# Kernel optimization log

Measured on AMD Instinct MI355X. Metric: run time of the kernel, lower is better.

The kernel has to match this reference:

```python
import jax, jax.numpy as jnp
import numpy as np

N_NODES = 50000
N_EDGES = 800000
NF = 64       # input_nf = output_nf = hidden_nf
RADIAL = 1

def tanhshrink(x):
    return x - jnp.tanh(x)

def _linear_params(key, fan_in, fan_out):
    k1, k2 = jax.random.split(key)
    s = 1.0 / np.sqrt(fan_in)
    W = jax.random.uniform(k1, (fan_in, fan_out), jnp.float32, -s, s)
    b = jax.random.uniform(k2, (fan_out,), jnp.float32, -s, s)
    return W, b

def setup_inputs() -> dict:
    key = jax.random.key(0)
    ks = jax.random.split(key, 11)
    nodes = jax.random.normal(ks[0], (N_NODES, NF), jnp.float32)
    coord = jax.random.normal(ks[1], (N_NODES, 3), jnp.float32)
    edges = jax.random.randint(ks[2], (2, N_EDGES), 0, N_NODES, jnp.int64)
    # Edge MLP: Linear(2*NF + RADIAL -> NF), Linear(NF -> NF)
    eW1, eb1 = _linear_params(ks[3], 2 * NF + RADIAL, NF)
    eW2, eb2 = _linear_params(ks[4], NF, NF)
    # Edge attention: Linear(2*NF -> NF), Linear(NF -> 1)
    aW1, ab1 = _linear_params(ks[5], 2 * NF, NF)
    aW2, ab2 = _linear_params(ks[6], NF, 1)
    # Node MLP: Linear(NF + NF -> NF), Linear(NF -> NF)
    nW1, nb1 = _linear_params(ks[7], 2 * NF, NF)
    nW2, nb2 = _linear_params(ks[8], NF, NF)
    # Coord MLP: Linear(NF -> NF), Linear(NF -> 1)
    cW1, cb1 = _linear_params(ks[9], NF, NF)
    cW2, cb2 = _linear_params(ks[10], NF, 1)
    return dict(nodes=nodes, coord=coord, edges=edges,
                eW1=eW1, eb1=eb1, eW2=eW2, eb2=eb2,
                aW1=aW1, ab1=ab1, aW2=aW2, ab2=ab2,
                nW1=nW1, nb1=nb1, nW2=nW2, nb2=nb2,
                cW1=cW1, cb1=cb1, cW2=cW2, cb2=cb2)

def reference(nodes, coord, edges,
              eW1, eb1, eW2, eb2,
              aW1, ab1, aW2, ab2,
              nW1, nb1, nW2, nb2,
              cW1, cb1, cW2, cb2):
    row, col = edges[0], edges[1]
    n = nodes.shape[0]
    # Radial: squared distance along each edge
    rij = coord[row] - coord[col]                       # [E, 3]
    radial = jnp.sum(rij * rij, axis=1, keepdims=True)  # [E, 1]
    src, tgt = nodes[row], nodes[col]                   # [E, NF]
    # Edge MLP with attention gate
    agg_in = jnp.concatenate([src, tgt, radial], axis=1)
    h = tanhshrink(agg_in @ eW1 + eb1)
    h = tanhshrink(h @ eW2 + eb2)                       # [E, NF]
    att_in = jnp.concatenate([src, tgt], axis=1)
    a = tanhshrink(att_in @ aW1 + ab1)
    a = jax.nn.sigmoid(a @ aW2 + ab2)                   # [E, 1]
    edge_feat = h * a                                   # [E, NF]
    # Coordinate update: rij scaled by scalar per edge, scatter-add to row
    c = tanhshrink(edge_feat @ cW1 + cb1)
    trans = rij * (c @ cW2 + cb2)                       # [E, 3]
    coord_out = coord + jax.ops.segment_sum(trans, row, num_segments=n)
    # Node update: scatter-add edge features to row, residual MLP
    agg = jax.ops.segment_sum(edge_feat, row, num_segments=n)  # [N, NF]
    m = jnp.concatenate([nodes, agg], axis=1)
    m = tanhshrink(m @ nW1 + nb1)
    nodes_out = nodes + (m @ nW2 + nb2)
    return nodes_out, coord_out
```

## Files before the change

### kernel.cpp

```cpp
#include <hip/hip_runtime.h>
#include <hip/hip_fp16.h>

#define NF 64

typedef _Float16 half8 __attribute__((ext_vector_type(8)));
typedef float f32x4 __attribute__((ext_vector_type(4)));

__device__ __forceinline__ float ts_f(float x){
  float t = __expf(2.0f*x);
  float th = 1.0f - 2.0f*__builtin_amdgcn_rcpf(t + 1.0f);
  return x - th;
}
__device__ __forceinline__ float sigmoid_f(float x){
  return __builtin_amdgcn_rcpf(1.0f + __expf(-x));
}

__global__ __launch_bounds__(256) void k_prepw_hist(
    const float* __restrict__ eW1, const float* __restrict__ aW1,
    const float* __restrict__ eW2, const float* __restrict__ cW1,
    const float* __restrict__ nW1, const float* __restrict__ nW2,
    _Float16* __restrict__ W256t, _Float16* __restrict__ N1t,
    _Float16* __restrict__ W2t, _Float16* __restrict__ C1t,
    _Float16* __restrict__ N2t,
    const int* __restrict__ edges, int* __restrict__ counts, int E)
{
  const int bi = blockIdx.x;
  if (bi < 64){
    const int t = bi*256 + threadIdx.x;
    {
      const int n = t >> 6, k = t & 63;
      float v;
      if      (n < 64)  v = eW1[k*NF + n];
      else if (n < 128) v = aW1[k*NF + (n-64)];
      else if (n < 192) v = eW1[(64+k)*NF + (n-128)];
      else              v = aW1[(64+k)*NF + (n-192)];
      W256t[t] = (_Float16)v;
    }
    if (t < 64*128){
      const int n = t >> 7, k = t & 127;
      N1t[t] = (_Float16)nW1[k*NF + n];
    }
    if (t < 64*64){
      const int n = t >> 6, k = t & 63;
      W2t[t] = (_Float16)eW2[k*NF + n];
      C1t[t] = (_Float16)cW1[k*NF + n];
      N2t[t] = (_Float16)nW2[k*NF + n];
    }
  } else {
    const int e = (bi - 64)*256 + threadIdx.x;
    if (e < E) atomicAdd(&counts[edges[e]], 1);
  }
}

__global__ __launch_bounds__(256) void k_scan(
    const int* __restrict__ counts, int* __restrict__ offs,
    int* __restrict__ btot, int* __restrict__ btop, int* __restrict__ done)
{
  __shared__ int s[256];
  __shared__ int isLast;
  const int t = threadIdx.x;
  const int b = blockIdx.x;

  const int4 c = *(const int4*)(counts + b*1024 + 4*t);
  const int mysum = c.x + c.y + c.z + c.w;
  s[t] = mysum; __syncthreads();
  #pragma unroll
  for (int d=1; d<256; d<<=1){
    const int v = (t>=d) ? s[t-d] : 0; __syncthreads();
    s[t] += v; __syncthreads();
  }
  const int base = (t==0) ? 0 : s[t-1];
  int4 o;
  o.x = base; o.y = base + c.x; o.z = o.y + c.y; o.w = o.z + c.z;
  *(int4*)(offs + b*1024 + 4*t) = o;
  if (t == 255) btot[b] = s[255];

  __threadfence();
  if (t == 0) isLast = (atomicAdd(done, 1) == (int)gridDim.x - 1);
  __syncthreads();
  if (isLast){
    __threadfence();
    const int nb = gridDim.x;
    const int v = (t < nb) ? btot[t] : 0;
    s[t] = v; __syncthreads();
    #pragma unroll
    for (int d=1; d<256; d<<=1){
      const int u = (t>=d) ? s[t-d] : 0; __syncthreads();
      s[t] += u; __syncthreads();
    }
    if (t < nb) btop[t] = (t==0) ? 0 : s[t-1];
  }
}

__global__ __launch_bounds__(64, 8) void k_pre_scatter(
    const float* __restrict__ nodes,
    const float* __restrict__ eb1, const float* __restrict__ ab1,
    const _Float16* __restrict__ W256t,
    _Float16* __restrict__ P, _Float16* __restrict__ Q, int N,
    const int* __restrict__ edges, int* __restrict__ offs,
    const int* __restrict__ btop, int2* __restrict__ ecomb, int E,
    int preBlocks)
{
  const int bi = blockIdx.x;
  const int lane = threadIdx.x;
  if (bi >= preBlocks){
    const int e = (bi - preBlocks)*64 + lane;
    if (e < E){
      const int r = edges[e], c = edges[E + e];
      const int pos = btop[r >> 10] + atomicAdd(&offs[r], 1);
      ecomb[pos] = make_int2(r, c);
    }
    return;
  }

  const int p = lane & 15, q = lane >> 4;
  const int m0 = bi * 16;
  const int row = m0 + p;

  const float* __restrict__ xr = nodes + (size_t)row * NF;
  half8 A[2];
  #pragma unroll
  for (int kt=0; kt<2; kt++){
    const float4 xa = *(const float4*)(xr + kt*32 + q*8);
    const float4 xb = *(const float4*)(xr + kt*32 + q*8 + 4);
    A[kt][0]=(_Float16)xa.x; A[kt][1]=(_Float16)xa.y; A[kt][2]=(_Float16)xa.z; A[kt][3]=(_Float16)xa.w;
    A[kt][4]=(_Float16)xb.x; A[kt][5]=(_Float16)xb.y; A[kt][6]=(_Float16)xb.z; A[kt][7]=(_Float16)xb.w;
  }

  #pragma unroll
  for (int ni=0; ni<16; ni++){
    float b = 0.f;
    if (ni < 4)       b = eb1[16*ni + p];
    else if (ni < 8)  b = ab1[16*(ni-4) + p];
    f32x4 acc = (f32x4){b,b,b,b};
    #pragma unroll
    for (int kt=0; kt<2; kt++){
      const half8 Bf = *(const half8*)(W256t + (size_t)(16*ni + p)*NF + kt*32 + q*8);
      acc = __builtin_amdgcn_mfma_f32_16x16x32_f16(A[kt], Bf, acc, 0,0,0);
    }
    _Float16* __restrict__ dst = (ni < 8 ? P : Q);
    const int colbase = (ni & 7) * 16 + p;
    #pragma unroll
    for (int rr=0; rr<4; rr++)
      dst[(size_t)(m0 + 4*q + rr)*128 + colbase] = (_Float16)acc[rr];
  }
}

__global__ __launch_bounds__(64, 4) void egcl_edge(
    const float* __restrict__ coord,
    const int2*  __restrict__ ecomb,
    const _Float16* __restrict__ P, const _Float16* __restrict__ Q,
    const float* __restrict__ eW1,
    const _Float16* __restrict__ W2t, const float* __restrict__ eb2,
    const float* __restrict__ aW2, const float* __restrict__ ab2,
    const _Float16* __restrict__ C1t, const float* __restrict__ cb1,
    const float* __restrict__ cW2, const float* __restrict__ cb2,
    _Float16* __restrict__ aggh, float* __restrict__ coord_out,
    int E)
{
  __shared__ _Float16 tile[64][72];
  __shared__ float gbuf[64];
  __shared__ float csbuf[64];
  __shared__ float tbuf[64][4];
  __shared__ int   rbuf[64];

  const int lane = threadIdx.x;
  const int p = lane & 15, q = lane >> 4;
  const int e = blockIdx.x * 64 + lane;
  const bool valid = (e < E);
  const int el = valid ? e : (E - 1);

  const int2 e2 = ecomb[el];
  const int r = e2.x, c = e2.y;
  rbuf[lane] = valid ? r : -1;

  const float rx = coord[3*r+0] - coord[3*c+0];
  const float ry = coord[3*r+1] - coord[3*c+1];
  const float rz = coord[3*r+2] - coord[3*c+2];
  const float radial = rx*rx + ry*ry + rz*rz;

  const _Float16* __restrict__ Pr = P + (size_t)r * 128;
  const _Float16* __restrict__ Qc = Q + (size_t)c * 128;
  const float* __restrict__ wrad = eW1 + 128*NF;

  half8 Bf[4][2];
  #pragma unroll
  for (int ni=0;ni<4;ni++)
    #pragma unroll
    for (int kt=0;kt<2;kt++)
      Bf[ni][kt] = *(const half8*)(W2t + (size_t)(16*ni + p)*NF + kt*32 + q*8);

  float sp0=0.f, sp1=0.f;
  #pragma unroll
  for (int g=0;g<8;g++){
    const half8 pa = *(const half8*)(Pr + 64 + 8*g);
    const half8 qa = *(const half8*)(Qc + 64 + 8*g);
    #pragma unroll
    for (int j=0;j<8;j++){
      const float v = ts_f((float)pa[j] + (float)qa[j]);
      if (j & 1) sp1 = fmaf(v, aW2[8*g+j], sp1); else sp0 = fmaf(v, aW2[8*g+j], sp0);
    }
  }
  const float gate = sigmoid_f(sp0 + sp1 + ab2[0]);
  gbuf[lane] = gate;

  #pragma unroll
  for (int g=0;g<8;g++){
    const half8 ph = *(const half8*)(Pr + 8*g);
    const half8 qh = *(const half8*)(Qc + 8*g);
    half8 hv;
    #pragma unroll
    for (int j=0;j<8;j++)
      hv[j] = (_Float16)ts_f(fmaf(radial, wrad[8*g+j], (float)ph[j] + (float)qh[j]));
    *(half8*)&tile[lane][8*g] = hv;
  }
  __syncthreads();

  f32x4 acc[4][4];
  #pragma unroll
  for (int ni=0;ni<4;ni++){
    const float b = eb2[16*ni + p];
    #pragma unroll
    for (int mi=0;mi<4;mi++) acc[mi][ni] = (f32x4){b,b,b,b};
  }
  #pragma unroll
  for (int mi=0;mi<4;mi++){
    #pragma unroll
    for (int kt=0;kt<2;kt++){
      const half8 Af = *(const half8*)&tile[16*mi + p][kt*32 + q*8];
      #pragma unroll
      for (int ni=0;ni<4;ni++)
        acc[mi][ni] = __builtin_amdgcn_mfma_f32_16x16x32_f16(Af, Bf[ni][kt], acc[mi][ni], 0,0,0);
    }
  }
  __syncthreads();

  #pragma unroll
  for (int mi=0;mi<4;mi++){
    #pragma unroll
    for (int rr=0;rr<4;rr++){
      const int row = 16*mi + 4*q + rr;
      const float gv = gbuf[row];
      #pragma unroll
      for (int ni=0;ni<4;ni++)
        tile[row][16*ni + p] = (_Float16)(ts_f(acc[mi][ni][rr]) * gv);
    }
  }

  #pragma unroll
  for (int ni=0;ni<4;ni++)
    #pragma unroll
    for (int kt=0;kt<2;kt++)
      Bf[ni][kt] = *(const half8*)(C1t + (size_t)(16*ni + p)*NF + kt*32 + q*8);
  #pragma unroll
  for (int ni=0;ni<4;ni++){
    const float b = cb1[16*ni + p];
    #pragma unroll
    for (int mi=0;mi<4;mi++) acc[mi][ni] = (f32x4){b,b,b,b};
  }
  __syncthreads();
  #pragma unroll
  for (int mi=0;mi<4;mi++){
    #pragma unroll
    for (int kt=0;kt<2;kt++){
      const half8 Af = *(const half8*)&tile[16*mi + p][kt*32 + q*8];
      #pragma unroll
      for (int ni=0;ni<4;ni++)
        acc[mi][ni] = __builtin_amdgcn_mfma_f32_16x16x32_f16(Af, Bf[ni][kt], acc[mi][ni], 0,0,0);
    }
  }

  float part[4][4];
  {
    float w2c[4];
    #pragma unroll
    for (int ni=0;ni<4;ni++) w2c[ni] = cW2[16*ni + p];
    #pragma unroll
    for (int mi=0;mi<4;mi++)
      #pragma unroll
      for (int rr=0;rr<4;rr++){
        float s = 0.f;
        #pragma unroll
        for (int ni=0;ni<4;ni++) s = fmaf(ts_f(acc[mi][ni][rr]), w2c[ni], s);
        part[mi][rr] = s;
      }
  }
  #pragma unroll
  for (int mask=1; mask<16; mask<<=1)
    #pragma unroll
    for (int mi=0;mi<4;mi++)
      #pragma unroll
      for (int rr=0;rr<4;rr++)
        part[mi][rr] += __shfl_xor(part[mi][rr], mask);
  {
    float v = 0.f;
    #pragma unroll
    for (int mi=0;mi<4;mi++)
      #pragma unroll
      for (int rr=0;rr<4;rr++)
        if (((p>>2)==mi) & ((p&3)==rr)) v = part[mi][rr];
    csbuf[16*(p>>2) + 4*q + (p&3)] = v + cb2[0];
  }
  __syncthreads();

  {
    const float cse = csbuf[lane];
    tbuf[lane][0] = rx * cse;
    tbuf[lane][1] = ry * cse;
    tbuf[lane][2] = rz * cse;
  }
  __syncthreads();

  {
    int cur = rbuf[0];
    float runsum = 0.f, rc = 0.f;
    #pragma unroll 1
    for (int eo=0; eo<64; eo++){
      const int rr2 = rbuf[eo];
      if (rr2 != cur){
        const float v0 = __shfl(runsum, 2*lane);
        const float v1 = __shfl(runsum, 2*lane+1);
        if (cur >= 0){
          if (lane < 32){
            __half2 hv; hv.x = __float2half(v0); hv.y = __float2half(v1);
            unsafeAtomicAdd((__half2*)aggh + (size_t)cur*32 + lane, hv);
          }
          if (lane < 3) atomicAdd(coord_out + 3*cur + lane, rc);
        }
        runsum = 0.f; rc = 0.f; cur = rr2;
      }
      runsum += (float)tile[eo][lane];
      if (lane < 3) rc += tbuf[eo][lane];
    }
    const float v0 = __shfl(runsum, 2*lane);
    const float v1 = __shfl(runsum, 2*lane+1);
    if (cur >= 0){
      if (lane < 32){
        __half2 hv; hv.x = __float2half(v0); hv.y = __float2half(v1);
        unsafeAtomicAdd((__half2*)aggh + (size_t)cur*32 + lane, hv);
      }
      if (lane < 3) atomicAdd(coord_out + 3*cur + lane, rc);
    }
  }
}

__global__ __launch_bounds__(64, 8) void egcl_node(
    const float* __restrict__ nodes, const float* __restrict__ coord,
    const _Float16* __restrict__ aggh,
    const _Float16* __restrict__ N1t, const float* __restrict__ nb1,
    const _Float16* __restrict__ N2t, const float* __restrict__ nb2,
    float* __restrict__ out_nodes, float* __restrict__ out_coord, int N)
{
  __shared__ _Float16 t2[16][72];
  const int lane = threadIdx.x;
  const int p = lane & 15, q = lane >> 4;
  const int m0 = blockIdx.x * 16;
  const int row = m0 + p;

  half8 A[4];
  const float* __restrict__ xr = nodes + (size_t)row * NF;
  #pragma unroll
  for (int kt=0; kt<2; kt++){
    const float4 xa = *(const float4*)(xr + kt*32 + q*8);
    const float4 xb = *(const float4*)(xr + kt*32 + q*8 + 4);
    A[kt][0]=(_Float16)xa.x; A[kt][1]=(_Float16)xa.y; A[kt][2]=(_Float16)xa.z; A[kt][3]=(_Float16)xa.w;
    A[kt][4]=(_Float16)xb.x; A[kt][5]=(_Float16)xb.y; A[kt][6]=(_Float16)xb.z; A[kt][7]=(_Float16)xb.w;
  }
  const _Float16* __restrict__ ar = aggh + (size_t)row * NF;
  #pragma unroll
  for (int kt=2; kt<4; kt++)
    A[kt] = *(const half8*)(ar + (kt-2)*32 + q*8);

  f32x4 acc[4];
  #pragma unroll
  for (int ni=0;ni<4;ni++){
    const float b = nb1[16*ni + p];
    acc[ni] = (f32x4){b,b,b,b};
  }
  #pragma unroll
  for (int kt=0; kt<4; kt++){
    #pragma unroll
    for (int ni=0;ni<4;ni++){
      const half8 Bf = *(const half8*)(N1t + (size_t)(16*ni + p)*128 + kt*32 + q*8);
      acc[ni] = __builtin_amdgcn_mfma_f32_16x16x32_f16(A[kt], Bf, acc[ni], 0,0,0);
    }
  }

  #pragma unroll
  for (int ni=0;ni<4;ni++)
    #pragma unroll
    for (int rr=0;rr<4;rr++)
      t2[4*q + rr][16*ni + p] = (_Float16)ts_f(acc[ni][rr]);
  __syncthreads();

  half8 A2[2];
  #pragma unroll
  for (int kt=0; kt<2; kt++)
    A2[kt] = *(const half8*)&t2[p][kt*32 + q*8];

  f32x4 acc2[4];
  #pragma unroll
  for (int ni=0;ni<4;ni++){
    const float b = nb2[16*ni + p];
    acc2[ni] = (f32x4){b,b,b,b};
  }
  #pragma unroll
  for (int kt=0; kt<2; kt++){
    #pragma unroll
    for (int ni=0;ni<4;ni++){
      const half8 Bf = *(const half8*)(N2t + (size_t)(16*ni + p)*NF + kt*32 + q*8);
      acc2[ni] = __builtin_amdgcn_mfma_f32_16x16x32_f16(A2[kt], Bf, acc2[ni], 0,0,0);
    }
  }

  #pragma unroll
  for (int ni=0;ni<4;ni++){
    #pragma unroll
    for (int rr=0;rr<4;rr++){
      const size_t idx = (size_t)(m0 + 4*q + rr)*NF + 16*ni + p;
      out_nodes[idx] = nodes[idx] + acc2[ni][rr];
    }
  }

  if (lane < 48)
    out_coord[(size_t)m0*3 + lane] += coord[(size_t)m0*3 + lane];
}

extern "C" void kernel_launch(void* const* d_in, const int* in_sizes, int n_in,
                              void* d_out, int out_size, void* d_ws, size_t ws_size,
                              hipStream_t stream)
{
  const float* nodes = (const float*)d_in[0];
  const float* coord = (const float*)d_in[1];
  const int*   edges = (const int*)  d_in[2];
  const float* eW1 = (const float*)d_in[3];
  const float* eb1 = (const float*)d_in[4];
  const float* eW2 = (const float*)d_in[5];
  const float* eb2 = (const float*)d_in[6];
  const float* aW1 = (const float*)d_in[7];
  const float* ab1 = (const float*)d_in[8];
  const float* aW2 = (const float*)d_in[9];
  const float* ab2 = (const float*)d_in[10];
  const float* nW1 = (const float*)d_in[11];
  const float* nb1 = (const float*)d_in[12];
  const float* nW2 = (const float*)d_in[13];
  const float* nb2 = (const float*)d_in[14];
  const float* cW1 = (const float*)d_in[15];
  const float* cb1 = (const float*)d_in[16];
  const float* cW2 = (const float*)d_in[17];
  const float* cb2 = (const float*)d_in[18];

  const int E = in_sizes[2] / 2;
  const int N = in_sizes[0] / NF;
  const int SCAN_B = (N + 1023) >> 10;
  const int NBINS  = SCAN_B << 10;
  float* out_nodes = (float*)d_out;
  float* out_coord = out_nodes + (size_t)N * NF;

  char* w = (char*)d_ws;
  _Float16* P     = (_Float16*)w;  w += (size_t)N * 128 * 2;
  _Float16* Qh    = (_Float16*)w;  w += (size_t)N * 128 * 2;
  char* zbase = w;
  _Float16* aggh  = (_Float16*)w;  w += (size_t)N * 64 * 2;
  int* counts     = (int*)w;       w += (size_t)NBINS * 4;
  int* done       = (int*)w;       w += 256;
  const size_t zlen = (size_t)(w - zbase);
  int* offs       = (int*)w;       w += (size_t)NBINS * 4;
  int* btot       = (int*)w;       w += 256*4;
  int* btop       = (int*)w;       w += 256*4;
  int2* ecomb     = (int2*)w;      w += (size_t)E * 8;
  _Float16* W256t = (_Float16*)w;  w += 256*64*2;
  _Float16* N1t   = (_Float16*)w;  w += 64*128*2;
  _Float16* W2t   = (_Float16*)w;  w += 64*64*2;
  _Float16* C1t   = (_Float16*)w;  w += 64*64*2;
  _Float16* N2t   = (_Float16*)w;  w += 64*64*2;

  hipMemsetAsync(out_coord, 0, (size_t)N * 3 * sizeof(float), stream);
  hipMemsetAsync(zbase, 0, zlen, stream);

  const int histBlocks = (E + 255)/256;
  k_prepw_hist<<<64 + histBlocks, 256, 0, stream>>>(eW1, aW1, eW2, cW1, nW1, nW2,
      W256t, N1t, W2t, C1t, N2t, edges, counts, E);

  k_scan<<<SCAN_B, 256, 0, stream>>>(counts, offs, btot, btop, done);

  const int preBlocks = (N + 15)/16;
  const int scatBlocks = (E + 63)/64;
  k_pre_scatter<<<preBlocks + scatBlocks, 64, 0, stream>>>(nodes, eb1, ab1, W256t,
      P, Qh, N, edges, offs, btop, ecomb, E, preBlocks);

  egcl_edge<<<(E + 63)/64, 64, 0, stream>>>(coord, ecomb, P, Qh,
      eW1, W2t, eb2, aW2, ab2, C1t, cb1, cW2, cb2,
      aggh, out_coord, E);

  egcl_node<<<(N + 15)/16, 64, 0, stream>>>(nodes, coord, aggh,
      N1t, nb1, N2t, nb2, out_nodes, out_coord, N);
}
```

Measured before the change: 343.4 us.

## Reuse histogram atomic ranks for edge scatter and fold zeroing into scan

The histogram pass now records each edge's atomicAdd return value as its rank within its row. The scatter pass then computes the sorted position as block offset + row offset + rank, with no second contended atomic. The aggregation buffer and coord_out are zeroed by extra blocks of the scan kernel instead of a separate memset. The sorted edge list is also split from int2 into separate row and column arrays. The cost is an extra E-sized rank array that must be written and read back.

Result: faster. 305.5 us (-11.1%).

```diff
diff --git a/kernel.cpp b/kernel.cpp
--- a/kernel.cpp
+++ b/kernel.cpp
@@ -22,7 +22,8 @@
     _Float16* __restrict__ W256t, _Float16* __restrict__ N1t,
     _Float16* __restrict__ W2t, _Float16* __restrict__ C1t,
     _Float16* __restrict__ N2t,
-    const int* __restrict__ edges, int* __restrict__ counts, int E)
+    const int* __restrict__ edges, int* __restrict__ counts,
+    int* __restrict__ rank, int E)
 {
   const int bi = blockIdx.x;
   if (bi < 64){
@@ -48,19 +49,30 @@
     }
   } else {
     const int e = (bi - 64)*256 + threadIdx.x;
-    if (e < E) atomicAdd(&counts[edges[e]], 1);
-  }
-}
-
-__global__ __launch_bounds__(256) void k_scan(
+    if (e < E) rank[e] = atomicAdd(&counts[edges[e]], 1);
+  }
+}
+
+__global__ __launch_bounds__(256) void k_scan_zero(
     const int* __restrict__ counts, int* __restrict__ offs,
-    int* __restrict__ btot, int* __restrict__ btop, int* __restrict__ done)
+    int* __restrict__ btot, int* __restrict__ btop, int* __restrict__ done,
+    float4* __restrict__ zagg, int naggf4,
+    float4* __restrict__ zcoord, int ncoordf4,
+    int SCAN_B)
 {
+  const int t = threadIdx.x;
+  const int b = blockIdx.x;
+  if (b >= SCAN_B){
+    const float4 z = make_float4(0.f,0.f,0.f,0.f);
+    const int nthr = (gridDim.x - SCAN_B) * 256;
+    const int tid = (b - SCAN_B)*256 + t;
+    for (int i = tid; i < naggf4; i += nthr)   zagg[i] = z;
+    for (int i = tid; i < ncoordf4; i += nthr) zcoord[i] = z;
+    return;
+  }
+
   __shared__ int s[256];
   __shared__ int isLast;
-  const int t = threadIdx.x;
-  const int b = blockIdx.x;
-
   const int4 c = *(const int4*)(counts + b*1024 + 4*t);
   const int mysum = c.x + c.y + c.z + c.w;
   s[t] = mysum; __syncthreads();
@@ -76,19 +88,18 @@
   if (t == 255) btot[b] = s[255];
 
   __threadfence();
-  if (t == 0) isLast = (atomicAdd(done, 1) == (int)gridDim.x - 1);
+  if (t == 0) isLast = (atomicAdd(done, 1) == SCAN_B - 1);
   __syncthreads();
   if (isLast){
     __threadfence();
-    const int nb = gridDim.x;
-    const int v = (t < nb) ? btot[t] : 0;
+    const int v = (t < SCAN_B) ? btot[t] : 0;
     s[t] = v; __syncthreads();
     #pragma unroll
     for (int d=1; d<256; d<<=1){
       const int u = (t>=d) ? s[t-d] : 0; __syncthreads();
       s[t] += u; __syncthreads();
     }
-    if (t < nb) btop[t] = (t==0) ? 0 : s[t-1];
+    if (t < SCAN_B) btop[t] = (t==0) ? 0 : s[t-1];
   }
 }
 
@@ -97,8 +108,9 @@
     const float* __restrict__ eb1, const float* __restrict__ ab1,
     const _Float16* __restrict__ W256t,
     _Float16* __restrict__ P, _Float16* __restrict__ Q, int N,
-    const int* __restrict__ edges, int* __restrict__ offs,
-    const int* __restrict__ btop, int2* __restrict__ ecomb, int E,
+    const int* __restrict__ edges, const int* __restrict__ offs,
+    const int* __restrict__ btop, const int* __restrict__ rank,
+    int* __restrict__ rs, int* __restrict__ cs, int E,
     int preBlocks)
 {
   const int bi = blockIdx.x;
@@ -107,8 +119,8 @@
     const int e = (bi - preBlocks)*64 + lane;
     if (e < E){
       const int r = edges[e], c = edges[E + e];
-      const int pos = btop[r >> 10] + atomicAdd(&offs[r], 1);
-      ecomb[pos] = make_int2(r, c);
+      const int pos = btop[r >> 10] + offs[r] + rank[e];
+      rs[pos] = r; cs[pos] = c;
     }
     return;
   }
@@ -148,7 +160,7 @@
 
 __global__ __launch_bounds__(64, 4) void egcl_edge(
     const float* __restrict__ coord,
-    const int2*  __restrict__ ecomb,
+    const int*   __restrict__ rs, const int* __restrict__ cs,
     const _Float16* __restrict__ P, const _Float16* __restrict__ Q,
     const float* __restrict__ eW1,
     const _Float16* __restrict__ W2t, const float* __restrict__ eb2,
@@ -170,8 +182,8 @@
   const bool valid = (e < E);
   const int el = valid ? e : (E - 1);
 
-  const int2 e2 = ecomb[el];
-  const int r = e2.x, c = e2.y;
+  const int r = rs[el];
+  const int c = cs[el];
   rbuf[lane] = valid ? r : -1;
 
   const float rx = coord[3*r+0] - coord[3*c+0];
@@ -460,36 +472,40 @@
   char* w = (char*)d_ws;
   _Float16* P     = (_Float16*)w;  w += (size_t)N * 128 * 2;
   _Float16* Qh    = (_Float16*)w;  w += (size_t)N * 128 * 2;
+  _Float16* aggh  = (_Float16*)w;  w += (size_t)N * 64 * 2;
   char* zbase = w;
-  _Float16* aggh  = (_Float16*)w;  w += (size_t)N * 64 * 2;
   int* counts     = (int*)w;       w += (size_t)NBINS * 4;
   int* done       = (int*)w;       w += 256;
   const size_t zlen = (size_t)(w - zbase);
   int* offs       = (int*)w;       w += (size_t)NBINS * 4;
   int* btot       = (int*)w;       w += 256*4;
   int* btop       = (int*)w;       w += 256*4;
-  int2* ecomb     = (int2*)w;      w += (size_t)E * 8;
+  int* rank       = (int*)w;       w += (size_t)E * 4;
+  int* rs         = (int*)w;       w += (size_t)E * 4;
+  int* cs_        = (int*)w;       w += (size_t)E * 4;
   _Float16* W256t = (_Float16*)w;  w += 256*64*2;
   _Float16* N1t   = (_Float16*)w;  w += 64*128*2;
   _Float16* W2t   = (_Float16*)w;  w += 64*64*2;
   _Float16* C1t   = (_Float16*)w;  w += 64*64*2;
   _Float16* N2t   = (_Float16*)w;  w += 64*64*2;
 
-  hipMemsetAsync(out_coord, 0, (size_t)N * 3 * sizeof(float), stream);
   hipMemsetAsync(zbase, 0, zlen, stream);
 
   const int histBlocks = (E + 255)/256;
   k_prepw_hist<<<64 + histBlocks, 256, 0, stream>>>(eW1, aW1, eW2, cW1, nW1, nW2,
-      W256t, N1t, W2t, C1t, N2t, edges, counts, E);
-
-  k_scan<<<SCAN_B, 256, 0, stream>>>(counts, offs, btot, btop, done);
+      W256t, N1t, W2t, C1t, N2t, edges, counts, rank, E);
+
+  const int naggf4   = (int)((size_t)N * 64 * 2 / 16);
+  const int ncoordf4 = (N * 3) / 4;
+  k_scan_zero<<<SCAN_B + 256, 256, 0, stream>>>(counts, offs, btot, btop, done,
+      (float4*)aggh, naggf4, (float4*)out_coord, ncoordf4, SCAN_B);
 
   const int preBlocks = (N + 15)/16;
   const int scatBlocks = (E + 63)/64;
   k_pre_scatter<<<preBlocks + scatBlocks, 64, 0, stream>>>(nodes, eb1, ab1, W256t,
-      P, Qh, N, edges, offs, btop, ecomb, E, preBlocks);
-
-  egcl_edge<<<(E + 63)/64, 64, 0, stream>>>(coord, ecomb, P, Qh,
+      P, Qh, N, edges, offs, btop, rank, rs, cs_, E, preBlocks);
+
+  egcl_edge<<<(E + 63)/64, 64, 0, stream>>>(coord, rs, cs_, P, Qh,
       eW1, W2t, eb2, aW2, ab2, C1t, cb1, cW2, cb2,
       aggh, out_coord, E);
 
```
